# Performance work log

Measured on AMD Instinct MI355X. Metric: run time of the kernel, lower is better.

The kernel has to match this reference:

```python
import jax, jax.numpy as jnp
import numpy as np

N = 40000      # nodes
E = 640000     # edges
F_IN = 128     # feature_dim
HID = 256      # hidden_dim
OUT = 128      # out_dim
B = 64         # num graphs
HEADS = 4
EPS = 1e-5


def setup_inputs() -> dict:
    key = jax.random.key(0)
    ks = jax.random.split(key, 32)
    s = 0.02
    inp = {
        "x_bb_masked": jax.random.normal(ks[0], (N, F_IN), jnp.float32),
        "x_att_masked": jax.random.normal(ks[1], (N, F_IN), jnp.float32),
        # SAGEConv1: in->hid  (lin_l acts on mean-aggregated neighbors, lin_r on root)
        "W1l": jax.random.normal(ks[2], (HID, F_IN), jnp.float32) * s,
        "b1l": jnp.zeros((HID,), jnp.float32),
        "W1r": jax.random.normal(ks[3], (HID, F_IN), jnp.float32) * s,
        # SAGEConv2: hid->hid
        "W2l": jax.random.normal(ks[4], (HID, HID), jnp.float32) * s,
        "b2l": jnp.zeros((HID,), jnp.float32),
        "W2r": jax.random.normal(ks[5], (HID, HID), jnp.float32) * s,
        # SAGEConv3: hid->out
        "W3l": jax.random.normal(ks[6], (OUT, HID), jnp.float32) * s,
        "b3l": jnp.zeros((OUT,), jnp.float32),
        "W3r": jax.random.normal(ks[7], (OUT, HID), jnp.float32) * s,
        # cross-attention projections
        "Wq": jax.random.normal(ks[8], (HID, F_IN), jnp.float32) * s,
        "bq": jnp.zeros((HID,), jnp.float32),
        "Wk": jax.random.normal(ks[9], (HID, OUT), jnp.float32) * s,
        "bk": jnp.zeros((HID,), jnp.float32),
        "Wv": jax.random.normal(ks[10], (HID, OUT), jnp.float32) * s,
        "bv": jnp.zeros((HID,), jnp.float32),
        # nn.MultiheadAttention packed in-proj and out-proj
        "in_proj_w": jax.random.normal(ks[11], (3 * HID, HID), jnp.float32) * s,
        "in_proj_b": jnp.zeros((3 * HID,), jnp.float32),
        "out_w": jax.random.normal(ks[12], (HID, HID), jnp.float32) * s,
        "out_b": jnp.zeros((HID,), jnp.float32),
        "ln_g": jnp.ones((HID,), jnp.float32),
        "ln_b": jnp.zeros((HID,), jnp.float32),
        "edge_index": jax.random.randint(ks[13], (2, E), 0, N, jnp.int64),
        "batch": jnp.sort(jax.random.randint(ks[14], (N,), 0, B, jnp.int64)),
    }
    return inp


def _sage(x, src, dst, Wl, bl, Wr):
    # mean aggregation of source features at target nodes, then lin_l(agg)+lin_r(x)
    agg = jax.ops.segment_sum(x[src], dst, num_segments=N)          # [N, d]
    cnt = jax.ops.segment_sum(jnp.ones((src.shape[0],), x.dtype), dst, num_segments=N)
    mean = agg / jnp.maximum(cnt, 1.0)[:, None]
    return mean @ Wl.T + bl + x @ Wr.T


def _forward(x_bb_masked, x_att_masked,
             W1l, b1l, W1r, W2l, b2l, W2r, W3l, b3l, W3r,
             Wq, bq, Wk, bk, Wv, bv, in_proj_w, in_proj_b, out_w, out_b,
             ln_g, ln_b, edge_index, batch):
    src, dst = edge_index[0], edge_index[1]
    h = jax.nn.relu(_sage(x_bb_masked, src, dst, W1l, b1l, W1r))
    h = jax.nn.relu(_sage(h, src, dst, W2l, b2l, W2r))
    h = _sage(h, src, dst, W3l, b3l, W3r)                           # [N, OUT]
    # global mean pool per graph
    gsum = jax.ops.segment_sum(h, batch, num_segments=B)            # [B, OUT]
    gcnt = jax.ops.segment_sum(jnp.ones((N,), h.dtype), batch, num_segments=B)
    graph_vec = gsum / jnp.maximum(gcnt, 1.0)[:, None]

    # cross attention: query per node, key/value from its graph vector (seq_len = 1)
    query = x_att_masked @ Wq.T + bq                                # [N, HID]
    gv = graph_vec[batch]                                           # [N, OUT]
    keyt = gv @ Wk.T + bk
    val = gv @ Wv.T + bv
    q = query @ in_proj_w[:HID].T + in_proj_b[:HID]
    k = keyt @ in_proj_w[HID:2 * HID].T + in_proj_b[HID:2 * HID]
    v = val @ in_proj_w[2 * HID:].T + in_proj_b[2 * HID:]
    dh = HID // HEADS
    qh = q.reshape(N, HEADS, dh)
    kh = k.reshape(N, HEADS, dh)
    vh = v.reshape(N, HEADS, dh)
    scores = jnp.sum(qh * kh, axis=-1, keepdims=True) / jnp.sqrt(jnp.asarray(dh, q.dtype))
    w = jax.nn.softmax(scores, axis=-1)                             # length-1 kv -> ones
    attn = (w * vh).reshape(N, HID)
    attn = attn @ out_w.T + out_b
    # LayerNorm
    mu = jnp.mean(attn, axis=-1, keepdims=True)
    var = jnp.mean((attn - mu) ** 2, axis=-1, keepdims=True)
    node_embeddings = (attn - mu) / jnp.sqrt(var + EPS) * ln_g + ln_b
    return graph_vec, node_embeddings


def reference(x_bb_masked, x_att_masked,
              W1l, b1l, W1r, W2l, b2l, W2r, W3l, b3l, W3r,
              Wq, bq, Wk, bk, Wv, bv, in_proj_w, in_proj_b, out_w, out_b,
              ln_g, ln_b, edge_index, batch):
    return _forward(x_bb_masked, x_att_masked,
                    W1l, b1l, W1r, W2l, b2l, W2r, W3l, b3l, W3r,
                    Wq, bq, Wk, bk, Wv, bv, in_proj_w, in_proj_b, out_w, out_b,
                    ln_g, ln_b, edge_index, batch)
```

## Files before the change

### kernel.cpp

```cpp
#include <hip/hip_runtime.h>

#define N_NODES 40000
#define N_EDGES 640000
#define NGRAPH 64

typedef unsigned short u16;
typedef unsigned int u32;
typedef __attribute__((ext_vector_type(4))) float floatx4;
typedef __attribute__((ext_vector_type(8))) short short8;
typedef __attribute__((ext_vector_type(8))) __bf16 bf16x8;

__device__ __forceinline__ float bf2f(u16 u) {
  u32 x = ((u32)u) << 16;
  return __builtin_bit_cast(float, x);
}
__device__ __forceinline__ u16 f2bf(float f) {
  u32 u = __builtin_bit_cast(u32, f);
  u += 0x7fffu + ((u >> 16) & 1u);
  return (u16)(u >> 16);
}
__device__ __forceinline__ void gld16(const void* g, void* l) {
  __builtin_amdgcn_global_load_lds(
      (const __attribute__((address_space(1))) u32*)g,
      (__attribute__((address_space(3))) u32*)l, 16, 0, 0);
}

__global__ void k_zero(int* p, int n) {
  int i = blockIdx.x * 256 + threadIdx.x;
  if (i < n) p[i] = 0;
}
__global__ void k_hist(const int* __restrict__ ei, int* __restrict__ cnt) {
  int e = blockIdx.x * 256 + threadIdx.x;
  int d = ei[N_EDGES + e];
  atomicAdd(&cnt[d], 1);
}
__global__ void k_blocksum(const int* __restrict__ cnt, int* __restrict__ bsum, int n) {
  __shared__ int s[256];
  int t = threadIdx.x, i = blockIdx.x * 256 + t;
  s[t] = (i < n) ? cnt[i] : 0;
  __syncthreads();
  for (int off = 128; off > 0; off >>= 1) {
    if (t < off) s[t] += s[t + off];
    __syncthreads();
  }
  if (t == 0) bsum[blockIdx.x] = s[0];
}
__global__ void k_scan_small(int* bsum, int n) {
  __shared__ int s[256];
  int t = threadIdx.x;
  int orig = (t < n) ? bsum[t] : 0;
  s[t] = orig;
  __syncthreads();
  for (int off = 1; off < 256; off <<= 1) {
    int v = (t >= off) ? s[t - off] : 0;
    __syncthreads();
    s[t] += v;
    __syncthreads();
  }
  if (t < n) bsum[t] = s[t] - orig;
}
__global__ void k_rowptr(const int* __restrict__ cnt, const int* __restrict__ bsum,
                         int* __restrict__ rowptr, float* __restrict__ invc, int n, int total) {
  __shared__ int s[256];
  int t = threadIdx.x, i = blockIdx.x * 256 + t;
  int c = (i < n) ? cnt[i] : 0;
  s[t] = c;
  __syncthreads();
  for (int off = 1; off < 256; off <<= 1) {
    int v = (t >= off) ? s[t - off] : 0;
    __syncthreads();
    s[t] += v;
    __syncthreads();
  }
  if (i < n) {
    rowptr[i] = bsum[blockIdx.x] + s[t] - c;
    invc[i] = 1.0f / (float)(c > 1 ? c : 1);
  }
  if (i == 0) rowptr[n] = total;
}
__global__ void k_scatter(const int* __restrict__ ei, const int* __restrict__ rowptr,
                          int* __restrict__ cursor, int* __restrict__ perm) {
  int e = blockIdx.x * 256 + threadIdx.x;
  int d = ei[N_EDGES + e];
  int srcn = ei[e];
  int pos = rowptr[d] + atomicAdd(&cursor[d], 1);
  perm[pos] = srcn;
}
__global__ void k_gstart(const int* __restrict__ batch, int* __restrict__ gstart) {
  int t = threadIdx.x;
  if (t <= NGRAPH) {
    int lo = 0, hi = N_NODES;
    while (lo < hi) { int mid = (lo + hi) >> 1; if (batch[mid] < t) lo = mid + 1; else hi = mid; }
    gstart[t] = lo;
  }
}

__global__ void k_f2b(const float* __restrict__ in, u16* __restrict__ out, int n4) {
  int i = blockIdx.x * 256 + threadIdx.x;
  if (i < n4) {
    float4 v = ((const float4*)in)[i];
    u32 lo = (u32)f2bf(v.x) | ((u32)f2bf(v.y) << 16);
    u32 hi = (u32)f2bf(v.z) | ((u32)f2bf(v.w) << 16);
    ((uint2*)out)[i] = make_uint2(lo, hi);
  }
}
__global__ void k_f2b6(const float* __restrict__ s0, u16* __restrict__ d0,
                       const float* __restrict__ s1, u16* __restrict__ d1,
                       const float* __restrict__ s2, u16* __restrict__ d2,
                       const float* __restrict__ s3, u16* __restrict__ d3,
                       const float* __restrict__ s4, u16* __restrict__ d4,
                       const float* __restrict__ s5, u16* __restrict__ d5) {
  int i = blockIdx.x * 256 + threadIdx.x;
  const float* s; u16* d; int off;
  if (i < 8192)       { s = s0; d = d0; off = i; }
  else if (i < 16384) { s = s1; d = d1; off = i - 8192; }
  else if (i < 32768) { s = s2; d = d2; off = i - 16384; }
  else if (i < 49152) { s = s3; d = d3; off = i - 32768; }
  else if (i < 57344) { s = s4; d = d4; off = i - 49152; }
  else                { s = s5; d = d5; off = i - 57344; }
  float4 v = ((const float4*)s)[off];
  u32 lo = (u32)f2bf(v.x) | ((u32)f2bf(v.y) << 16);
  u32 hi = (u32)f2bf(v.z) | ((u32)f2bf(v.w) << 16);
  ((uint2*)(d))[off] = make_uint2(lo, hi);
}

template <int D, int MODE>
__global__ __launch_bounds__(256) void k_agg(const u16* __restrict__ x, u16* __restrict__ outp,
                                             const int* __restrict__ rowptr,
                                             const int* __restrict__ perm,
                                             const float* __restrict__ invc,
                                             const u16* __restrict__ Radd, int nn) {
  constexpr int CW = D / 2;
  constexpr int LPR = CW / 8;
  constexpr int SLOTS = 64 / LPR;
  int wv = threadIdx.x >> 6, lane = threadIdx.x & 63;
  int node = blockIdx.x * 4 + wv;
  if (node >= nn) return;
  int s = rowptr[node], e = rowptr[node + 1];
  int slot = lane / LPR, lsub = lane % LPR;
  float acc[8];
#pragma unroll
  for (int i = 0; i < 8; ++i) acc[i] = 0.f;
  const u16* xl = x + blockIdx.y * CW + lsub * 8;

  int p = s + slot;
  for (; p + SLOTS < e; p += 2 * SLOTS) {
    int s0 = perm[p], s1 = perm[p + SLOTS];
    uint4 a = *(const uint4*)(xl + (size_t)s0 * D);
    uint4 b = *(const uint4*)(xl + (size_t)s1 * D);
    u32 wa[4] = {a.x, a.y, a.z, a.w}, wb[4] = {b.x, b.y, b.z, b.w};
#pragma unroll
    for (int j = 0; j < 4; ++j) {
      acc[2 * j] += __builtin_bit_cast(float, wa[j] << 16) + __builtin_bit_cast(float, wb[j] << 16);
      acc[2 * j + 1] += __builtin_bit_cast(float, wa[j] & 0xffff0000u) + __builtin_bit_cast(float, wb[j] & 0xffff0000u);
    }
  }
  for (; p < e; p += SLOTS) {
    int src = perm[p];
    uint4 a = *(const uint4*)(xl + (size_t)src * D);
    u32 wa[4] = {a.x, a.y, a.z, a.w};
#pragma unroll
    for (int j = 0; j < 4; ++j) {
      acc[2 * j] += __builtin_bit_cast(float, wa[j] << 16);
      acc[2 * j + 1] += __builtin_bit_cast(float, wa[j] & 0xffff0000u);
    }
  }

#pragma unroll
  for (int i = 0; i < 8; ++i) {
    if (SLOTS == 8) acc[i] += __shfl_xor(acc[i], 8, 64);
    acc[i] += __shfl_xor(acc[i], 16, 64);
    acc[i] += __shfl_xor(acc[i], 32, 64);
  }

  if (slot == 0) {
    float iv = invc[node];
    float v[8];
#pragma unroll
    for (int i = 0; i < 8; ++i) v[i] = acc[i] * iv;
    if (MODE == 1) {
      uint4 a = *(const uint4*)(Radd + (size_t)node * D + blockIdx.y * CW + lsub * 8);
      u32 wa[4] = {a.x, a.y, a.z, a.w};
#pragma unroll
      for (int j = 0; j < 4; ++j) {
        v[2 * j] += __builtin_bit_cast(float, wa[j] << 16);
        v[2 * j + 1] += __builtin_bit_cast(float, wa[j] & 0xffff0000u);
      }
    }
    u32 wpk[4];
#pragma unroll
    for (int i = 0; i < 4; ++i)
      wpk[i] = (u32)f2bf(v[2 * i]) | ((u32)f2bf(v[2 * i + 1]) << 16);
    *(uint4*)(outp + (size_t)node * D + blockIdx.y * CW + lsub * 8) =
        make_uint4(wpk[0], wpk[1], wpk[2], wpk[3]);
  }
}

template <int OUTW, int EPI>
__global__ __launch_bounds__(256) void k_gemm(const u16* __restrict__ A1, const u16* __restrict__ W1, int K1,
                                              const u16* __restrict__ A2, const u16* __restrict__ W2, int K2,
                                              const float* __restrict__ bias,
                                              u16* __restrict__ out1, u16* __restrict__ out2, int M) {
  __shared__ u16 lsA[128 * 64];
  __shared__ u16 lsB[128 * 64];
  const int tid = threadIdx.x, lane = tid & 63, wv = tid >> 6;
  const int wm = wv >> 1, wn = wv & 1;
  const int row0 = blockIdx.x * 128, col0 = blockIdx.y * 128;

  floatx4 acc[4][4];
#pragma unroll
  for (int r = 0; r < 4; ++r)
#pragma unroll
    for (int c = 0; c < 4; ++c) acc[r][c] = 0.f;

  for (int seg = 0; seg < 2; ++seg) {
    const u16* A = seg ? A2 : A1;
    const u16* Wm = seg ? W2 : W1;
    const int K = seg ? K2 : K1;
    if (K == 0) continue;
    for (int k0 = 0; k0 < K; k0 += 64) {
      __syncthreads();
#pragma unroll
      for (int i = 0; i < 4; ++i) {
        int chunk = i * 256 + tid;
        int r = chunk >> 3;
        int kc = chunk & 7;
        int kcs = kc ^ (r & 7);
        int grow = row0 + r;
        grow = grow < M ? grow : M - 1;
        gld16(A + (size_t)grow * K + (k0 + kcs * 8), lsA + (size_t)(i * 256 + wv * 64) * 8);
        int wr = col0 + r;
        gld16(Wm + (size_t)wr * K + (k0 + kcs * 8), lsB + (size_t)(i * 256 + wv * 64) * 8);
      }
      __syncthreads();
#pragma unroll
      for (int kk = 0; kk < 2; ++kk) {
        bf16x8 af[4], bb[4];
        int kc = kk * 4 + (lane >> 4);
#pragma unroll
        for (int r = 0; r < 4; ++r) {
          int row = wm * 64 + r * 16 + (lane & 15);
          af[r] = __builtin_bit_cast(bf16x8, *(const short8*)(lsA + row * 64 + ((kc ^ (row & 7)) << 3)));
        }
#pragma unroll
        for (int c = 0; c < 4; ++c) {
          int row = wn * 64 + c * 16 + (lane & 15);
          bb[c] = __builtin_bit_cast(bf16x8, *(const short8*)(lsB + row * 64 + ((kc ^ (row & 7)) << 3)));
        }
#pragma unroll
        for (int r = 0; r < 4; ++r)
#pragma unroll
          for (int c = 0; c < 4; ++c)
            acc[r][c] = __builtin_amdgcn_mfma_f32_16x16x32_bf16(af[r], bb[c], acc[r][c], 0, 0, 0);
      }
    }
  }

#pragma unroll
  for (int r = 0; r < 4; ++r) {
    int rowb = row0 + wm * 64 + r * 16 + ((lane >> 4) << 2);
#pragma unroll
    for (int c = 0; c < 4; ++c) {
      int col = col0 + wn * 64 + c * 16 + (lane & 15);
#pragma unroll
      for (int j = 0; j < 4; ++j) {
        int gr = rowb + j;
        if (gr < M) {
          float v = acc[r][c][j];
          if (EPI == 0) {
            v += bias[col];
            v = v > 0.f ? v : 0.f;
            out1[(size_t)gr * OUTW + col] = f2bf(v);
          } else {
            if (col < 128) {
              out1[(size_t)gr * 128 + col] = f2bf(v);
            } else {
              v += bias[col - 128];
              out2[(size_t)gr * 128 + (col - 128)] = f2bf(v);
            }
          }
        }
      }
    }
  }
}

__global__ __launch_bounds__(256) void k_pool_part(const u16* __restrict__ h3,
                                                   const int* __restrict__ batch,
                                                   float* __restrict__ gsum) {
  __shared__ int sb[64];
  int t = threadIdx.x;
  int n0 = blockIdx.x * 64;
  if (t < 64) sb[t] = batch[n0 + t];
  __syncthreads();
  int col = t & 127, sub = t >> 7;
  float acc = 0.f;
  int curg = -1;
  for (int i = sub; i < 64; i += 2) {
    int g = sb[i];
    if (g != curg) {
      if (curg >= 0) atomicAdd(&gsum[curg * 128 + col], acc);
      curg = g;
      acc = 0.f;
    }
    acc += bf2f(h3[(size_t)(n0 + i) * 128 + col]);
  }
  if (curg >= 0) atomicAdd(&gsum[curg * 128 + col], acc);
}

__global__ __launch_bounds__(256) void k_tail(const float* __restrict__ gsum, const int* __restrict__ gstart,
                                              const float* __restrict__ Wv,
                                              const float* __restrict__ bv, const float* __restrict__ ipw,
                                              const float* __restrict__ ipb, const float* __restrict__ outw,
                                              const float* __restrict__ outb, const float* __restrict__ lng,
                                              const float* __restrict__ lnb, float* __restrict__ dout,
                                              float* __restrict__ eout) {
  __shared__ float sa[256], sb[256];
  __shared__ float s_mu, s_var;
  int b = blockIdx.x, t = threadIdx.x;
  if (t < 128) {
    int cg = gstart[b + 1] - gstart[b];
    float mean = gsum[b * 128 + t] / (float)(cg > 1 ? cg : 1);
    sa[t] = mean;
    dout[b * 128 + t] = mean;
  }
  __syncthreads();
  float val = bv[t];
  for (int k = 0; k < 128; ++k) val += sa[k] * Wv[t * 128 + k];
  sb[t] = val;
  __syncthreads();
  float vv = ipb[512 + t];
  for (int k = 0; k < 256; ++k) vv += sb[k] * ipw[(size_t)(512 + t) * 256 + k];
  sa[t] = vv;
  __syncthreads();
  float at = outb[t];
  for (int k = 0; k < 256; ++k) at += sa[k] * outw[t * 256 + k];
  sb[t] = at;
  __syncthreads();
  for (int off = 128; off > 0; off >>= 1) {
    if (t < off) sb[t] += sb[t + off];
    __syncthreads();
  }
  if (t == 0) s_mu = sb[0] * (1.0f / 256.0f);
  __syncthreads();
  float d = at - s_mu;
  sb[t] = d * d;
  __syncthreads();
  for (int off = 128; off > 0; off >>= 1) {
    if (t < off) sb[t] += sb[t + off];
    __syncthreads();
  }
  if (t == 0) s_var = sb[0] * (1.0f / 256.0f);
  __syncthreads();
  float r = 1.0f / sqrtf(s_var + 1e-5f);
  eout[(size_t)b * 256 + t] = d * r * lng[t] + lnb[t];
}

__global__ void k_scat_out(const float* __restrict__ eb, const int* __restrict__ batch,
                           float* __restrict__ dout) {
  int i = blockIdx.x * 256 + threadIdx.x;
  int n = i >> 6, q = i & 63;
  float4 v = ((const float4*)eb)[(size_t)batch[n] * 64 + q];
  ((float4*)(dout + NGRAPH * 128))[i] = v;
}

extern "C" void kernel_launch(void* const* d_in, const int* in_sizes, int n_in,
                              void* d_out, int out_size, void* d_ws, size_t ws_size,
                              hipStream_t stream) {
  (void)in_sizes; (void)n_in; (void)out_size; (void)ws_size;
  const float* x_bb = (const float*)d_in[0];
  const float* W1l = (const float*)d_in[2];
  const float* b1l = (const float*)d_in[3];
  const float* W1r = (const float*)d_in[4];
  const float* W2l = (const float*)d_in[5];
  const float* b2l = (const float*)d_in[6];
  const float* W2r = (const float*)d_in[7];
  const float* W3l = (const float*)d_in[8];
  const float* b3l = (const float*)d_in[9];
  const float* W3r = (const float*)d_in[10];
  const float* Wv = (const float*)d_in[15];
  const float* bv = (const float*)d_in[16];
  const float* ipw = (const float*)d_in[17];
  const float* ipb = (const float*)d_in[18];
  const float* outw = (const float*)d_in[19];
  const float* outb = (const float*)d_in[20];
  const float* lng = (const float*)d_in[21];
  const float* lnb = (const float*)d_in[22];
  const int* ei = (const int*)d_in[23];
  const int* batch = (const int*)d_in[24];
  float* dout = (float*)d_out;
  char* ws = (char*)d_ws;

  constexpr size_t O_W1L = 0;
  constexpr size_t O_W1R = O_W1L + 256 * 128 * 2;
  constexpr size_t O_W2L = O_W1R + 256 * 128 * 2;
  constexpr size_t O_W2R = O_W2L + 256 * 256 * 2;
  constexpr size_t O_W3L = O_W2R + 256 * 256 * 2;
  constexpr size_t O_W3R = O_W3L + 128 * 256 * 2;
  constexpr size_t O_XB = O_W3R + 128 * 256 * 2;
  constexpr size_t O_MEAN1 = O_XB + (size_t)N_NODES * 128 * 2;
  constexpr size_t O_H1 = O_MEAN1 + (size_t)N_NODES * 128 * 2;
  constexpr size_t O_MEAN2 = O_H1 + (size_t)N_NODES * 256 * 2;
  constexpr size_t O_H2 = O_MEAN2 + (size_t)N_NODES * 256 * 2;
  constexpr size_t O_E = O_H2 + (size_t)N_NODES * 256 * 2;
  constexpr size_t O_CNT = O_E + 64 * 256 * 4;
  constexpr size_t O_CUR = O_CNT + (size_t)N_NODES * 4;
  constexpr size_t O_GSUM = O_CUR + (size_t)N_NODES * 4;
  constexpr size_t O_RP = O_GSUM + 64 * 128 * 4;
  constexpr size_t O_INVC = O_RP + (size_t)(N_NODES + 64) * 4;
  constexpr size_t O_BSUM = O_INVC + (size_t)N_NODES * 4;
  constexpr size_t O_GST = O_BSUM + 1024;
  constexpr size_t O_PERM = O_GST + 512;

  u16* w1l = (u16*)(ws + O_W1L);  u16* w1r = (u16*)(ws + O_W1R);
  u16* w2l = (u16*)(ws + O_W2L);  u16* w2r = (u16*)(ws + O_W2R);
  u16* w3s = (u16*)(ws + O_W3L);  u16* w3r = (u16*)(ws + O_W3R);
  u16* xb = (u16*)(ws + O_XB);
  u16* mean1 = (u16*)(ws + O_MEAN1);
  u16* h1 = (u16*)(ws + O_H1);
  u16* mean2 = (u16*)(ws + O_MEAN2);
  u16* h2 = (u16*)(ws + O_H2);
  u16* Pb = (u16*)(ws + O_XB);
  u16* Rb = (u16*)(ws + O_MEAN1);
  u16* h3b = (u16*)(ws + O_MEAN2);
  float* eb = (float*)(ws + O_E);
  int* cnt = (int*)(ws + O_CNT);
  int* cursor = (int*)(ws + O_CUR);
  float* gsum = (float*)(ws + O_GSUM);
  int* rowptr = (int*)(ws + O_RP);
  float* invc = (float*)(ws + O_INVC);
  int* bsum = (int*)(ws + O_BSUM);
  int* gstart = (int*)(ws + O_GST);
  int* perm = (int*)(ws + O_PERM);

  const int NB = (N_NODES + 255) / 256;

  k_zero<<<(2 * N_NODES + 8192 + 255) / 256, 256, 0, stream>>>(cnt, 2 * N_NODES + 8192);
  k_hist<<<N_EDGES / 256, 256, 0, stream>>>(ei, cnt);
  k_blocksum<<<NB, 256, 0, stream>>>(cnt, bsum, N_NODES);
  k_scan_small<<<1, 256, 0, stream>>>(bsum, NB);
  k_rowptr<<<NB, 256, 0, stream>>>(cnt, bsum, rowptr, invc, N_NODES, N_EDGES);
  k_scatter<<<N_EDGES / 256, 256, 0, stream>>>(ei, rowptr, cursor, perm);
  k_gstart<<<1, 128, 0, stream>>>(batch, gstart);

  k_f2b<<<(N_NODES * 128 / 4 + 255) / 256, 256, 0, stream>>>(x_bb, xb, N_NODES * 128 / 4);
  k_f2b6<<<256, 256, 0, stream>>>(W1l, w1l, W1r, w1r, W2l, w2l, W2r, w2r, W3l, w3s, W3r, w3r);

  dim3 blk(256);
  dim3 gagg(N_NODES / 4, 2);
  k_agg<128, 0><<<gagg, blk, 0, stream>>>(xb, mean1, rowptr, perm, invc, nullptr, N_NODES);
  k_gemm<256, 0><<<dim3(313, 2), blk, 0, stream>>>(mean1, w1l, 128, xb, w1r, 128, b1l, h1, nullptr, N_NODES);
  k_agg<256, 0><<<gagg, blk, 0, stream>>>(h1, mean2, rowptr, perm, invc, nullptr, N_NODES);
  k_gemm<256, 0><<<dim3(313, 2), blk, 0, stream>>>(mean2, w2l, 256, h1, w2r, 256, b2l, h2, nullptr, N_NODES);
  k_gemm<128, 3><<<dim3(313, 2), blk, 0, stream>>>(h2, w3s, 256, nullptr, nullptr, 0, b3l, Pb, Rb, N_NODES);
  k_agg<128, 1><<<gagg, blk, 0, stream>>>(Pb, h3b, rowptr, perm, invc, Rb, N_NODES);
  k_pool_part<<<N_NODES / 64, blk, 0, stream>>>(h3b, batch, gsum);
  k_tail<<<NGRAPH, blk, 0, stream>>>(gsum, gstart, Wv, bv, ipw, ipb, outw, outb, lng, lnb, dout, eb);
  k_scat_out<<<N_NODES * 64 / 256, blk, 0, stream>>>(eb, batch, dout);
}
```

Before: 317.0 us.

## Fuse preprocessing and tail stages into cooperative grid-synced kernels; widen agg rows

Replaces the chain of small CSR-build and conversion kernels with one cooperative kernel that uses grid-wide syncs between phases. Pool, tail MLP/LayerNorm and output scatter are likewise merged into a single cooperative kernel. The aggregation kernel now has one wave cover the full feature row (16 lanes per row, 4 edge slots) instead of splitting columns across a second grid dimension, which halves the number of index loads per row. The aim is to cut launch overhead and redundant perm reads, at the cost of grid.sync overhead and a fixed 512-block grid.

```diff
diff --git a/kernel.cpp b/kernel.cpp
--- a/kernel.cpp
+++ b/kernel.cpp
@@ -1,8 +1,12 @@
 #include <hip/hip_runtime.h>
+#include <hip/hip_cooperative_groups.h>
+
+namespace cg = cooperative_groups;
 
 #define N_NODES 40000
 #define N_EDGES 640000
 #define NGRAPH 64
+#define NBCH 157
 
 typedef unsigned short u16;
 typedef unsigned int u32;
@@ -19,109 +23,102 @@
   u += 0x7fffu + ((u >> 16) & 1u);
   return (u16)(u >> 16);
 }
+__device__ __forceinline__ uint2 f4tob(float4 v) {
+  u32 lo = (u32)f2bf(v.x) | ((u32)f2bf(v.y) << 16);
+  u32 hi = (u32)f2bf(v.z) | ((u32)f2bf(v.w) << 16);
+  return make_uint2(lo, hi);
+}
 __device__ __forceinline__ void gld16(const void* g, void* l) {
   __builtin_amdgcn_global_load_lds(
       (const __attribute__((address_space(1))) u32*)g,
       (__attribute__((address_space(3))) u32*)l, 16, 0, 0);
 }
 
-__global__ void k_zero(int* p, int n) {
-  int i = blockIdx.x * 256 + threadIdx.x;
-  if (i < n) p[i] = 0;
-}
-__global__ void k_hist(const int* __restrict__ ei, int* __restrict__ cnt) {
-  int e = blockIdx.x * 256 + threadIdx.x;
-  int d = ei[N_EDGES + e];
-  atomicAdd(&cnt[d], 1);
-}
-__global__ void k_blocksum(const int* __restrict__ cnt, int* __restrict__ bsum, int n) {
-  __shared__ int s[256];
-  int t = threadIdx.x, i = blockIdx.x * 256 + t;
-  s[t] = (i < n) ? cnt[i] : 0;
-  __syncthreads();
-  for (int off = 128; off > 0; off >>= 1) {
-    if (t < off) s[t] += s[t + off];
-    __syncthreads();
-  }
-  if (t == 0) bsum[blockIdx.x] = s[0];
-}
-__global__ void k_scan_small(int* bsum, int n) {
-  __shared__ int s[256];
-  int t = threadIdx.x;
-  int orig = (t < n) ? bsum[t] : 0;
-  s[t] = orig;
-  __syncthreads();
-  for (int off = 1; off < 256; off <<= 1) {
-    int v = (t >= off) ? s[t - off] : 0;
-    __syncthreads();
-    s[t] += v;
-    __syncthreads();
-  }
-  if (t < n) bsum[t] = s[t] - orig;
-}
-__global__ void k_rowptr(const int* __restrict__ cnt, const int* __restrict__ bsum,
-                         int* __restrict__ rowptr, float* __restrict__ invc, int n, int total) {
-  __shared__ int s[256];
-  int t = threadIdx.x, i = blockIdx.x * 256 + t;
-  int c = (i < n) ? cnt[i] : 0;
-  s[t] = c;
-  __syncthreads();
-  for (int off = 1; off < 256; off <<= 1) {
-    int v = (t >= off) ? s[t - off] : 0;
-    __syncthreads();
-    s[t] += v;
-    __syncthreads();
-  }
-  if (i < n) {
-    rowptr[i] = bsum[blockIdx.x] + s[t] - c;
-    invc[i] = 1.0f / (float)(c > 1 ? c : 1);
-  }
-  if (i == 0) rowptr[n] = total;
-}
-__global__ void k_scatter(const int* __restrict__ ei, const int* __restrict__ rowptr,
-                          int* __restrict__ cursor, int* __restrict__ perm) {
-  int e = blockIdx.x * 256 + threadIdx.x;
-  int d = ei[N_EDGES + e];
-  int srcn = ei[e];
-  int pos = rowptr[d] + atomicAdd(&cursor[d], 1);
-  perm[pos] = srcn;
-}
-__global__ void k_gstart(const int* __restrict__ batch, int* __restrict__ gstart) {
-  int t = threadIdx.x;
-  if (t <= NGRAPH) {
+struct PreArgs {
+  const float* x_bb;
+  const float *W1l, *W1r, *W2l, *W2r, *W3l, *W3r;
+  const int* ei;
+  const int* batch;
+  u16 *xb, *w1l, *w1r, *w2l, *w2r, *w3s, *w3r;
+  int* cnt;
+  int* cursor;
+  int* rowptr;
+  float* invc;
+  int* bsum;
+  int* gstart;
+  int* perm;
+};
+
+__global__ __launch_bounds__(256, 4) void k_pre(PreArgs a) {
+  cg::grid_group grid = cg::this_grid();
+  __shared__ int ssc[256];
+  const int t = threadIdx.x;
+  const int tid = blockIdx.x * 256 + t;
+  const int nth = gridDim.x * 256;
+
+  for (int i = tid; i < 2 * N_NODES + 8192; i += nth) a.cnt[i] = 0;
+  for (int i = tid; i < N_NODES * 32; i += nth)
+    ((uint2*)a.xb)[i] = f4tob(((const float4*)a.x_bb)[i]);
+  for (int i = tid; i < 65536; i += nth) {
+    const float* s; u16* d; int off;
+    if (i < 8192)       { s = a.W1l; d = a.w1l; off = i; }
+    else if (i < 16384) { s = a.W1r; d = a.w1r; off = i - 8192; }
+    else if (i < 32768) { s = a.W2l; d = a.w2l; off = i - 16384; }
+    else if (i < 49152) { s = a.W2r; d = a.w2r; off = i - 32768; }
+    else if (i < 57344) { s = a.W3l; d = a.w3s; off = i - 49152; }
+    else                { s = a.W3r; d = a.w3r; off = i - 57344; }
+    ((uint2*)d)[off] = f4tob(((const float4*)s)[off]);
+  }
+  grid.sync();
+  for (int e2 = tid; e2 < N_EDGES; e2 += nth)
+    atomicAdd(&a.cnt[a.ei[N_EDGES + e2]], 1);
+  grid.sync();
+  for (int c = blockIdx.x; c < NBCH; c += gridDim.x) {
+    int i = c * 256 + t;
+    int cv = (i < N_NODES) ? a.cnt[i] : 0;
+    ssc[t] = cv;
+    __syncthreads();
+    for (int off = 1; off < 256; off <<= 1) {
+      int v = (t >= off) ? ssc[t - off] : 0;
+      __syncthreads();
+      ssc[t] += v;
+      __syncthreads();
+    }
+    if (i < N_NODES) a.rowptr[i] = ssc[t] - cv;
+    if (t == 255) a.bsum[c] = ssc[255];
+    __syncthreads();
+  }
+  grid.sync();
+  if (blockIdx.x == 0) {
+    int orig = (t < NBCH) ? a.bsum[t] : 0;
+    ssc[t] = orig;
+    __syncthreads();
+    for (int off = 1; off < 256; off <<= 1) {
+      int v = (t >= off) ? ssc[t - off] : 0;
+      __syncthreads();
+      ssc[t] += v;
+      __syncthreads();
+    }
+    if (t < NBCH) a.bsum[t] = ssc[t] - orig;
+  }
+  grid.sync();
+  for (int i = tid; i < N_NODES; i += nth) {
+    int cv = a.cnt[i];
+    a.rowptr[i] += a.bsum[i >> 8];
+    a.invc[i] = 1.0f / (float)(cv > 1 ? cv : 1);
+  }
+  if (tid == 0) a.rowptr[N_NODES] = N_EDGES;
+  grid.sync();
+  for (int e2 = tid; e2 < N_EDGES; e2 += nth) {
+    int d = a.ei[N_EDGES + e2];
+    int pos = a.rowptr[d] + atomicAdd(&a.cursor[d], 1);
+    a.perm[pos] = a.ei[e2];
+  }
+  if (tid <= NGRAPH) {
     int lo = 0, hi = N_NODES;
-    while (lo < hi) { int mid = (lo + hi) >> 1; if (batch[mid] < t) lo = mid + 1; else hi = mid; }
-    gstart[t] = lo;
-  }
-}
-
-__global__ void k_f2b(const float* __restrict__ in, u16* __restrict__ out, int n4) {
-  int i = blockIdx.x * 256 + threadIdx.x;
-  if (i < n4) {
-    float4 v = ((const float4*)in)[i];
-    u32 lo = (u32)f2bf(v.x) | ((u32)f2bf(v.y) << 16);
-    u32 hi = (u32)f2bf(v.z) | ((u32)f2bf(v.w) << 16);
-    ((uint2*)out)[i] = make_uint2(lo, hi);
-  }
-}
-__global__ void k_f2b6(const float* __restrict__ s0, u16* __restrict__ d0,
-                       const float* __restrict__ s1, u16* __restrict__ d1,
-                       const float* __restrict__ s2, u16* __restrict__ d2,
-                       const float* __restrict__ s3, u16* __restrict__ d3,
-                       const float* __restrict__ s4, u16* __restrict__ d4,
-                       const float* __restrict__ s5, u16* __restrict__ d5) {
-  int i = blockIdx.x * 256 + threadIdx.x;
-  const float* s; u16* d; int off;
-  if (i < 8192)       { s = s0; d = d0; off = i; }
-  else if (i < 16384) { s = s1; d = d1; off = i - 8192; }
-  else if (i < 32768) { s = s2; d = d2; off = i - 16384; }
-  else if (i < 49152) { s = s3; d = d3; off = i - 32768; }
-  else if (i < 57344) { s = s4; d = d4; off = i - 49152; }
-  else                { s = s5; d = d5; off = i - 57344; }
-  float4 v = ((const float4*)s)[off];
-  u32 lo = (u32)f2bf(v.x) | ((u32)f2bf(v.y) << 16);
-  u32 hi = (u32)f2bf(v.z) | ((u32)f2bf(v.w) << 16);
-  ((uint2*)(d))[off] = make_uint2(lo, hi);
+    while (lo < hi) { int mid = (lo + hi) >> 1; if (a.batch[mid] < tid) lo = mid + 1; else hi = mid; }
+    a.gstart[tid] = lo;
+  }
 }
 
 template <int D, int MODE>
@@ -130,69 +127,97 @@
                                              const int* __restrict__ perm,
                                              const float* __restrict__ invc,
                                              const u16* __restrict__ Radd, int nn) {
-  constexpr int CW = D / 2;
-  constexpr int LPR = CW / 8;
-  constexpr int SLOTS = 64 / LPR;
   int wv = threadIdx.x >> 6, lane = threadIdx.x & 63;
   int node = blockIdx.x * 4 + wv;
   if (node >= nn) return;
   int s = rowptr[node], e = rowptr[node + 1];
-  int slot = lane / LPR, lsub = lane % LPR;
-  float acc[8];
-#pragma unroll
-  for (int i = 0; i < 8; ++i) acc[i] = 0.f;
-  const u16* xl = x + blockIdx.y * CW + lsub * 8;
+  int slot = lane >> 4, lsub = lane & 15;
+  constexpr int FR = D / 16;
+  float acc[FR];
+#pragma unroll
+  for (int i = 0; i < FR; ++i) acc[i] = 0.f;
+  const u16* xl = x + lsub * FR;
 
   int p = s + slot;
-  for (; p + SLOTS < e; p += 2 * SLOTS) {
-    int s0 = perm[p], s1 = perm[p + SLOTS];
-    uint4 a = *(const uint4*)(xl + (size_t)s0 * D);
-    uint4 b = *(const uint4*)(xl + (size_t)s1 * D);
-    u32 wa[4] = {a.x, a.y, a.z, a.w}, wb[4] = {b.x, b.y, b.z, b.w};
-#pragma unroll
-    for (int j = 0; j < 4; ++j) {
-      acc[2 * j] += __builtin_bit_cast(float, wa[j] << 16) + __builtin_bit_cast(float, wb[j] << 16);
-      acc[2 * j + 1] += __builtin_bit_cast(float, wa[j] & 0xffff0000u) + __builtin_bit_cast(float, wb[j] & 0xffff0000u);
-    }
-  }
-  for (; p < e; p += SLOTS) {
+  for (; p + 4 < e; p += 8) {
+    int src0 = perm[p];
+    int src1 = perm[p + 4];
+    const u16* rp0 = xl + (size_t)src0 * D;
+    const u16* rp1 = xl + (size_t)src1 * D;
+    if (D == 128) {
+      uint4 va = *(const uint4*)rp0;
+      uint4 vb = *(const uint4*)rp1;
+      u32 wa[4] = {va.x, va.y, va.z, va.w}, wb[4] = {vb.x, vb.y, vb.z, vb.w};
+#pragma unroll
+      for (int j = 0; j < 4; ++j) {
+        acc[2 * j] += __builtin_bit_cast(float, wa[j] << 16) + __builtin_bit_cast(float, wb[j] << 16);
+        acc[2 * j + 1] += __builtin_bit_cast(float, wa[j] & 0xffff0000u) + __builtin_bit_cast(float, wb[j] & 0xffff0000u);
+      }
+    } else {
+      uint4 a0 = *(const uint4*)rp0;
+      uint4 a1 = *(const uint4*)(rp0 + 8);
+      uint4 b0 = *(const uint4*)rp1;
+      uint4 b1 = *(const uint4*)(rp1 + 8);
+      u32 wa[8] = {a0.x, a0.y, a0.z, a0.w, a1.x, a1.y, a1.z, a1.w};
+      u32 wb[8] = {b0.x, b0.y, b0.z, b0.w, b1.x, b1.y, b1.z, b1.w};
+#pragma unroll
+      for (int j = 0; j < 8; ++j) {
+        acc[2 * j] += __builtin_bit_cast(float, wa[j] << 16) + __builtin_bit_cast(float, wb[j] << 16);
+        acc[2 * j + 1] += __builtin_bit_cast(float, wa[j] & 0xffff0000u) + __builtin_bit_cast(float, wb[j] & 0xffff0000u);
+      }
+    }
+  }
+  if (p < e) {
     int src = perm[p];
-    uint4 a = *(const uint4*)(xl + (size_t)src * D);
-    u32 wa[4] = {a.x, a.y, a.z, a.w};
-#pragma unroll
-    for (int j = 0; j < 4; ++j) {
-      acc[2 * j] += __builtin_bit_cast(float, wa[j] << 16);
-      acc[2 * j + 1] += __builtin_bit_cast(float, wa[j] & 0xffff0000u);
-    }
-  }
-
-#pragma unroll
-  for (int i = 0; i < 8; ++i) {
-    if (SLOTS == 8) acc[i] += __shfl_xor(acc[i], 8, 64);
+    const u16* rp = xl + (size_t)src * D;
+    if (D == 128) {
+      uint4 va = *(const uint4*)rp;
+      u32 wa[4] = {va.x, va.y, va.z, va.w};
+#pragma unroll
+      for (int j = 0; j < 4; ++j) {
+        acc[2 * j] += __builtin_bit_cast(float, wa[j] << 16);
+        acc[2 * j + 1] += __builtin_bit_cast(float, wa[j] & 0xffff0000u);
+      }
+    } else {
+      uint4 a0 = *(const uint4*)rp;
+      uint4 a1 = *(const uint4*)(rp + 8);
+      u32 wa[8] = {a0.x, a0.y, a0.z, a0.w, a1.x, a1.y, a1.z, a1.w};
+#pragma unroll
+      for (int j = 0; j < 8; ++j) {
+        acc[2 * j] += __builtin_bit_cast(float, wa[j] << 16);
+        acc[2 * j + 1] += __builtin_bit_cast(float, wa[j] & 0xffff0000u);
+      }
+    }
+  }
+
+#pragma unroll
+  for (int i = 0; i < FR; ++i) {
     acc[i] += __shfl_xor(acc[i], 16, 64);
     acc[i] += __shfl_xor(acc[i], 32, 64);
   }
 
   if (slot == 0) {
     float iv = invc[node];
-    float v[8];
-#pragma unroll
-    for (int i = 0; i < 8; ++i) v[i] = acc[i] * iv;
+    float v[FR];
+#pragma unroll
+    for (int i = 0; i < FR; ++i) v[i] = acc[i] * iv;
     if (MODE == 1) {
-      uint4 a = *(const uint4*)(Radd + (size_t)node * D + blockIdx.y * CW + lsub * 8);
-      u32 wa[4] = {a.x, a.y, a.z, a.w};
+      const uint4* rr = (const uint4*)(Radd + (size_t)node * D + lsub * FR);
+      uint4 va = rr[0];
+      u32 wa[4] = {va.x, va.y, va.z, va.w};
 #pragma unroll
       for (int j = 0; j < 4; ++j) {
         v[2 * j] += __builtin_bit_cast(float, wa[j] << 16);
         v[2 * j + 1] += __builtin_bit_cast(float, wa[j] & 0xffff0000u);
       }
     }
-    u32 wpk[4];
-#pragma unroll
-    for (int i = 0; i < 4; ++i)
+    u32 wpk[FR / 2];
+#pragma unroll
+    for (int i = 0; i < FR / 2; ++i)
       wpk[i] = (u32)f2bf(v[2 * i]) | ((u32)f2bf(v[2 * i + 1]) << 16);
-    *(uint4*)(outp + (size_t)node * D + blockIdx.y * CW + lsub * 8) =
-        make_uint4(wpk[0], wpk[1], wpk[2], wpk[3]);
+    uint4* o = (uint4*)(outp + (size_t)node * D + lsub * FR);
+    o[0] = make_uint4(wpk[0], wpk[1], wpk[2], wpk[3]);
+    if (FR == 16) o[1] = make_uint4(wpk[4], wpk[5], wpk[6], wpk[7]);
   }
 }
 
@@ -285,83 +310,89 @@
   }
 }
 
-__global__ __launch_bounds__(256) void k_pool_part(const u16* __restrict__ h3,
-                                                   const int* __restrict__ batch,
-                                                   float* __restrict__ gsum) {
-  __shared__ int sb[64];
-  int t = threadIdx.x;
-  int n0 = blockIdx.x * 64;
-  if (t < 64) sb[t] = batch[n0 + t];
-  __syncthreads();
-  int col = t & 127, sub = t >> 7;
-  float acc = 0.f;
-  int curg = -1;
-  for (int i = sub; i < 64; i += 2) {
-    int g = sb[i];
-    if (g != curg) {
-      if (curg >= 0) atomicAdd(&gsum[curg * 128 + col], acc);
-      curg = g;
-      acc = 0.f;
-    }
-    acc += bf2f(h3[(size_t)(n0 + i) * 128 + col]);
-  }
-  if (curg >= 0) atomicAdd(&gsum[curg * 128 + col], acc);
-}
-
-__global__ __launch_bounds__(256) void k_tail(const float* __restrict__ gsum, const int* __restrict__ gstart,
-                                              const float* __restrict__ Wv,
-                                              const float* __restrict__ bv, const float* __restrict__ ipw,
-                                              const float* __restrict__ ipb, const float* __restrict__ outw,
-                                              const float* __restrict__ outb, const float* __restrict__ lng,
-                                              const float* __restrict__ lnb, float* __restrict__ dout,
-                                              float* __restrict__ eout) {
+struct PostArgs {
+  const u16* h3;
+  const int* batch;
+  float* gsum;
+  const int* gstart;
+  const float *Wv, *bv, *ipw, *ipb, *outw, *outb, *lng, *lnb;
+  float* dout;
+  float* eout;
+};
+
+__global__ __launch_bounds__(256, 4) void k_post(PostArgs a) {
+  cg::grid_group grid = cg::this_grid();
   __shared__ float sa[256], sb[256];
+  __shared__ int sbi[64];
   __shared__ float s_mu, s_var;
-  int b = blockIdx.x, t = threadIdx.x;
-  if (t < 128) {
-    int cg = gstart[b + 1] - gstart[b];
-    float mean = gsum[b * 128 + t] / (float)(cg > 1 ? cg : 1);
-    sa[t] = mean;
-    dout[b * 128 + t] = mean;
-  }
-  __syncthreads();
-  float val = bv[t];
-  for (int k = 0; k < 128; ++k) val += sa[k] * Wv[t * 128 + k];
-  sb[t] = val;
-  __syncthreads();
-  float vv = ipb[512 + t];
-  for (int k = 0; k < 256; ++k) vv += sb[k] * ipw[(size_t)(512 + t) * 256 + k];
-  sa[t] = vv;
-  __syncthreads();
-  float at = outb[t];
-  for (int k = 0; k < 256; ++k) at += sa[k] * outw[t * 256 + k];
-  sb[t] = at;
-  __syncthreads();
-  for (int off = 128; off > 0; off >>= 1) {
-    if (t < off) sb[t] += sb[t + off];
-    __syncthreads();
-  }
-  if (t == 0) s_mu = sb[0] * (1.0f / 256.0f);
-  __syncthreads();
-  float d = at - s_mu;
-  sb[t] = d * d;
-  __syncthreads();
-  for (int off = 128; off > 0; off >>= 1) {
-    if (t < off) sb[t] += sb[t + off];
-    __syncthreads();
-  }
-  if (t == 0) s_var = sb[0] * (1.0f / 256.0f);
-  __syncthreads();
-  float r = 1.0f / sqrtf(s_var + 1e-5f);
-  eout[(size_t)b * 256 + t] = d * r * lng[t] + lnb[t];
-}
-
-__global__ void k_scat_out(const float* __restrict__ eb, const int* __restrict__ batch,
-                           float* __restrict__ dout) {
-  int i = blockIdx.x * 256 + threadIdx.x;
-  int n = i >> 6, q = i & 63;
-  float4 v = ((const float4*)eb)[(size_t)batch[n] * 64 + q];
-  ((float4*)(dout + NGRAPH * 128))[i] = v;
+  const int t = threadIdx.x;
+
+  for (int c = blockIdx.x; c < N_NODES / 64; c += gridDim.x) {
+    int n0 = c * 64;
+    if (t < 64) sbi[t] = a.batch[n0 + t];
+    __syncthreads();
+    int col = t & 127, sub = t >> 7;
+    float acc = 0.f;
+    int curg = -1;
+    for (int i = sub; i < 64; i += 2) {
+      int g = sbi[i];
+      if (g != curg) {
+        if (curg >= 0) atomicAdd(&a.gsum[curg * 128 + col], acc);
+        curg = g;
+        acc = 0.f;
+      }
+      acc += bf2f(a.h3[(size_t)(n0 + i) * 128 + col]);
+    }
+    if (curg >= 0) atomicAdd(&a.gsum[curg * 128 + col], acc);
+    __syncthreads();
+  }
+  grid.sync();
+  if (blockIdx.x < NGRAPH) {
+    int b = blockIdx.x;
+    if (t < 128) {
+      int cg2 = a.gstart[b + 1] - a.gstart[b];
+      float mean = a.gsum[b * 128 + t] / (float)(cg2 > 1 ? cg2 : 1);
+      sa[t] = mean;
+      a.dout[b * 128 + t] = mean;
+    }
+    __syncthreads();
+    float val = a.bv[t];
+    for (int k = 0; k < 128; ++k) val += sa[k] * a.Wv[t * 128 + k];
+    sb[t] = val;
+    __syncthreads();
+    float vv = a.ipb[512 + t];
+    for (int k = 0; k < 256; ++k) vv += sb[k] * a.ipw[(size_t)(512 + t) * 256 + k];
+    sa[t] = vv;
+    __syncthreads();
+    float at = a.outb[t];
+    for (int k = 0; k < 256; ++k) at += sa[k] * a.outw[t * 256 + k];
+    sb[t] = at;
+    __syncthreads();
+    for (int off = 128; off > 0; off >>= 1) {
+      if (t < off) sb[t] += sb[t + off];
+      __syncthreads();
+    }
+    if (t == 0) s_mu = sb[0] * (1.0f / 256.0f);
+    __syncthreads();
+    float d = at - s_mu;
+    sb[t] = d * d;
+    __syncthreads();
+    for (int off = 128; off > 0; off >>= 1) {
+      if (t < off) sb[t] += sb[t + off];
+      __syncthreads();
+    }
+    if (t == 0) s_var = sb[0] * (1.0f / 256.0f);
+    __syncthreads();
+    float r = 1.0f / sqrtf(s_var + 1e-5f);
+    a.eout[(size_t)b * 256 + t] = d * r * a.lng[t] + a.lnb[t];
+  }
+  grid.sync();
+  const int nth = gridDim.x * 256;
+  float4* od = (float4*)(a.dout + NGRAPH * 128);
+  for (int i = blockIdx.x * 256 + t; i < N_NODES * 64; i += nth) {
+    int n = i >> 6, q = i & 63;
+    od[i] = ((const float4*)a.eout)[(size_t)a.batch[n] * 64 + q];
+  }
 }
 
 extern "C" void kernel_launch(void* const* d_in, const int* in_sizes, int n_in,
@@ -433,28 +464,29 @@
   int* gstart = (int*)(ws + O_GST);
   int* perm = (int*)(ws + O_PERM);
 
-  const int NB = (N_NODES + 255) / 256;
-
-  k_zero<<<(2 * N_NODES + 8192 + 255) / 256, 256, 0, stream>>>(cnt, 2 * N_NODES + 8192);
-  k_hist<<<N_EDGES / 256, 256, 0, stream>>>(ei, cnt);
-  k_blocksum<<<NB, 256, 0, stream>>>(cnt, bsum, N_NODES);
-  k_scan_small<<<1, 256, 0, stream>>>(bsum, NB);
-  k_rowptr<<<NB, 256, 0, stream>>>(cnt, bsum, rowptr, invc, N_NODES, N_EDGES);
-  k_scatter<<<N_EDGES / 256, 256, 0, stream>>>(ei, rowptr, cursor, perm);
-  k_gstart<<<1, 128, 0, stream>>>(batch, gstart);
-
-  k_f2b<<<(N_NODES * 128 / 4 + 255) / 256, 256, 0, stream>>>(x_bb, xb, N_NODES * 128 / 4);
-  k_f2b6<<<256, 256, 0, stream>>>(W1l, w1l, W1r, w1r, W2l, w2l, W2r, w2r, W3l, w3s, W3r, w3r);
+  PreArgs pa;
+  pa.x_bb = x_bb; pa.W1l = W1l; pa.W1r = W1r; pa.W2l = W2l; pa.W2r = W2r;
+  pa.W3l = W3l; pa.W3r = W3r; pa.ei = ei; pa.batch = batch;
+  pa.xb = xb; pa.w1l = w1l; pa.w1r = w1r; pa.w2l = w2l; pa.w2r = w2r;
+  pa.w3s = w3s; pa.w3r = w3r;
+  pa.cnt = cnt; pa.cursor = cursor; pa.rowptr = rowptr; pa.invc = invc;
+  pa.bsum = bsum; pa.gstart = gstart; pa.perm = perm;
+  void* pargs[] = { &pa };
+  hipLaunchCooperativeKernel((void*)k_pre, dim3(512), dim3(256), pargs, 0, stream);
 
   dim3 blk(256);
-  dim3 gagg(N_NODES / 4, 2);
-  k_agg<128, 0><<<gagg, blk, 0, stream>>>(xb, mean1, rowptr, perm, invc, nullptr, N_NODES);
+  k_agg<128, 0><<<N_NODES / 4, blk, 0, stream>>>(xb, mean1, rowptr, perm, invc, nullptr, N_NODES);
   k_gemm<256, 0><<<dim3(313, 2), blk, 0, stream>>>(mean1, w1l, 128, xb, w1r, 128, b1l, h1, nullptr, N_NODES);
-  k_agg<256, 0><<<gagg, blk, 0, stream>>>(h1, mean2, rowptr, perm, invc, nullptr, N_NODES);
+  k_agg<256, 0><<<N_NODES / 4, blk, 0, stream>>>(h1, mean2, rowptr, perm, invc, nullptr, N_NODES);
   k_gemm<256, 0><<<dim3(313, 2), blk, 0, stream>>>(mean2, w2l, 256, h1, w2r, 256, b2l, h2, nullptr, N_NODES);
   k_gemm<128, 3><<<dim3(313, 2), blk, 0, stream>>>(h2, w3s, 256, nullptr, nullptr, 0, b3l, Pb, Rb, N_NODES);
-  k_agg<128, 1><<<gagg, blk, 0, stream>>>(Pb, h3b, rowptr, perm, invc, Rb, N_NODES);
-  k_pool_part<<<N_NODES / 64, blk, 0, stream>>>(h3b, batch, gsum);
-  k_tail<<<NGRAPH, blk, 0, stream>>>(gsum, gstart, Wv, bv, ipw, ipb, outw, outb, lng, lnb, dout, eb);
-  k_scat_out<<<N_NODES * 64 / 256, blk, 0, stream>>>(eb, batch, dout);
-}
+  k_agg<128, 1><<<N_NODES / 4, blk, 0, stream>>>(Pb, h3b, rowptr, perm, invc, Rb, N_NODES);
+
+  PostArgs qa;
+  qa.h3 = h3b; qa.batch = batch; qa.gsum = gsum; qa.gstart = gstart;
+  qa.Wv = Wv; qa.bv = bv; qa.ipw = ipw; qa.ipb = ipb;
+  qa.outw = outw; qa.outb = outb; qa.lng = lng; qa.lnb = lnb;
+  qa.dout = dout; qa.eout = eb;
+  void* qargs[] = { &qa };
+  hipLaunchCooperativeKernel((void*)k_post, dim3(512), dim3(256), qargs, 0, stream);
+}
```

Result: slower. 697.5 us (+120.1%).

## Merge setup kernels and process full feature rows per wave in aggregation

Applied to the files above, without the earlier changes.

Folds the zeroing, bf16 conversion of x and weights, and graph-start search into a single grid-stride setup kernel, cutting several launches. The aggregation kernel drops the two-way column split in blockIdx.y: each wave now covers the whole feature row with 16 lanes per row and 4 edge slots, loading 16 or 32 bytes per lane. Each edge index is read once instead of twice and the block count halves. The trade-off is fewer waves and more registers for the D=256 case, plus only 4 edges in flight per wave where D=128 previously had 8.

```diff
diff --git a/kernel.cpp b/kernel.cpp
--- a/kernel.cpp
+++ b/kernel.cpp
@@ -19,16 +19,48 @@
   u += 0x7fffu + ((u >> 16) & 1u);
   return (u16)(u >> 16);
 }
+__device__ __forceinline__ uint2 f4tob(float4 v) {
+  u32 lo = (u32)f2bf(v.x) | ((u32)f2bf(v.y) << 16);
+  u32 hi = (u32)f2bf(v.z) | ((u32)f2bf(v.w) << 16);
+  return make_uint2(lo, hi);
+}
 __device__ __forceinline__ void gld16(const void* g, void* l) {
   __builtin_amdgcn_global_load_lds(
       (const __attribute__((address_space(1))) u32*)g,
       (__attribute__((address_space(3))) u32*)l, 16, 0, 0);
 }
 
-__global__ void k_zero(int* p, int n) {
-  int i = blockIdx.x * 256 + threadIdx.x;
-  if (i < n) p[i] = 0;
-}
+__global__ __launch_bounds__(256) void k_setup(const float* __restrict__ x_bb, u16* __restrict__ xb,
+                                               const float* __restrict__ W1l, u16* __restrict__ w1l,
+                                               const float* __restrict__ W1r, u16* __restrict__ w1r,
+                                               const float* __restrict__ W2l, u16* __restrict__ w2l,
+                                               const float* __restrict__ W2r, u16* __restrict__ w2r,
+                                               const float* __restrict__ W3l, u16* __restrict__ w3s,
+                                               const float* __restrict__ W3r, u16* __restrict__ w3r,
+                                               int* __restrict__ zbase,
+                                               const int* __restrict__ batch, int* __restrict__ gstart) {
+  const int tid = blockIdx.x * 256 + threadIdx.x;
+  const int nth = gridDim.x * 256;
+  for (int i = tid; i < 2 * N_NODES + 8192; i += nth) zbase[i] = 0;
+  for (int i = tid; i < N_NODES * 32; i += nth)
+    ((uint2*)xb)[i] = f4tob(((const float4*)x_bb)[i]);
+  for (int i = tid; i < 65536; i += nth) {
+    const float* s; u16* d; int off;
+    if (i < 8192)       { s = W1l; d = w1l; off = i; }
+    else if (i < 16384) { s = W1r; d = w1r; off = i - 8192; }
+    else if (i < 32768) { s = W2l; d = w2l; off = i - 16384; }
+    else if (i < 49152) { s = W2r; d = w2r; off = i - 32768; }
+    else if (i < 57344) { s = W3l; d = w3s; off = i - 49152; }
+    else                { s = W3r; d = w3r; off = i - 57344; }
+    ((uint2*)d)[off] = f4tob(((const float4*)s)[off]);
+  }
+  if (tid <= NGRAPH) {
+    int lo = 0, hi = N_NODES;
+    while (lo < hi) { int mid = (lo + hi) >> 1; if (batch[mid] < tid) lo = mid + 1; else hi = mid; }
+    gstart[tid] = lo;
+  }
+}
+
 __global__ void k_hist(const int* __restrict__ ei, int* __restrict__ cnt) {
   int e = blockIdx.x * 256 + threadIdx.x;
   int d = ei[N_EDGES + e];
@@ -86,43 +118,6 @@
   int pos = rowptr[d] + atomicAdd(&cursor[d], 1);
   perm[pos] = srcn;
 }
-__global__ void k_gstart(const int* __restrict__ batch, int* __restrict__ gstart) {
-  int t = threadIdx.x;
-  if (t <= NGRAPH) {
-    int lo = 0, hi = N_NODES;
-    while (lo < hi) { int mid = (lo + hi) >> 1; if (batch[mid] < t) lo = mid + 1; else hi = mid; }
-    gstart[t] = lo;
-  }
-}
-
-__global__ void k_f2b(const float* __restrict__ in, u16* __restrict__ out, int n4) {
-  int i = blockIdx.x * 256 + threadIdx.x;
-  if (i < n4) {
-    float4 v = ((const float4*)in)[i];
-    u32 lo = (u32)f2bf(v.x) | ((u32)f2bf(v.y) << 16);
-    u32 hi = (u32)f2bf(v.z) | ((u32)f2bf(v.w) << 16);
-    ((uint2*)out)[i] = make_uint2(lo, hi);
-  }
-}
-__global__ void k_f2b6(const float* __restrict__ s0, u16* __restrict__ d0,
-                       const float* __restrict__ s1, u16* __restrict__ d1,
-                       const float* __restrict__ s2, u16* __restrict__ d2,
-                       const float* __restrict__ s3, u16* __restrict__ d3,
-                       const float* __restrict__ s4, u16* __restrict__ d4,
-                       const float* __restrict__ s5, u16* __restrict__ d5) {
-  int i = blockIdx.x * 256 + threadIdx.x;
-  const float* s; u16* d; int off;
-  if (i < 8192)       { s = s0; d = d0; off = i; }
-  else if (i < 16384) { s = s1; d = d1; off = i - 8192; }
-  else if (i < 32768) { s = s2; d = d2; off = i - 16384; }
-  else if (i < 49152) { s = s3; d = d3; off = i - 32768; }
-  else if (i < 57344) { s = s4; d = d4; off = i - 49152; }
-  else                { s = s5; d = d5; off = i - 57344; }
-  float4 v = ((const float4*)s)[off];
-  u32 lo = (u32)f2bf(v.x) | ((u32)f2bf(v.y) << 16);
-  u32 hi = (u32)f2bf(v.z) | ((u32)f2bf(v.w) << 16);
-  ((uint2*)(d))[off] = make_uint2(lo, hi);
-}
 
 template <int D, int MODE>
 __global__ __launch_bounds__(256) void k_agg(const u16* __restrict__ x, u16* __restrict__ outp,
@@ -130,69 +125,97 @@
                                              const int* __restrict__ perm,
                                              const float* __restrict__ invc,
                                              const u16* __restrict__ Radd, int nn) {
-  constexpr int CW = D / 2;
-  constexpr int LPR = CW / 8;
-  constexpr int SLOTS = 64 / LPR;
   int wv = threadIdx.x >> 6, lane = threadIdx.x & 63;
   int node = blockIdx.x * 4 + wv;
   if (node >= nn) return;
   int s = rowptr[node], e = rowptr[node + 1];
-  int slot = lane / LPR, lsub = lane % LPR;
-  float acc[8];
-#pragma unroll
-  for (int i = 0; i < 8; ++i) acc[i] = 0.f;
-  const u16* xl = x + blockIdx.y * CW + lsub * 8;
+  int slot = lane >> 4, lsub = lane & 15;
+  constexpr int FR = D / 16;
+  float acc[FR];
+#pragma unroll
+  for (int i = 0; i < FR; ++i) acc[i] = 0.f;
+  const u16* xl = x + lsub * FR;
 
   int p = s + slot;
-  for (; p + SLOTS < e; p += 2 * SLOTS) {
-    int s0 = perm[p], s1 = perm[p + SLOTS];
-    uint4 a = *(const uint4*)(xl + (size_t)s0 * D);
-    uint4 b = *(const uint4*)(xl + (size_t)s1 * D);
-    u32 wa[4] = {a.x, a.y, a.z, a.w}, wb[4] = {b.x, b.y, b.z, b.w};
-#pragma unroll
-    for (int j = 0; j < 4; ++j) {
-      acc[2 * j] += __builtin_bit_cast(float, wa[j] << 16) + __builtin_bit_cast(float, wb[j] << 16);
-      acc[2 * j + 1] += __builtin_bit_cast(float, wa[j] & 0xffff0000u) + __builtin_bit_cast(float, wb[j] & 0xffff0000u);
-    }
-  }
-  for (; p < e; p += SLOTS) {
+  for (; p + 4 < e; p += 8) {
+    int src0 = perm[p];
+    int src1 = perm[p + 4];
+    const u16* rp0 = xl + (size_t)src0 * D;
+    const u16* rp1 = xl + (size_t)src1 * D;
+    if (D == 128) {
+      uint4 va = *(const uint4*)rp0;
+      uint4 vb = *(const uint4*)rp1;
+      u32 wa[4] = {va.x, va.y, va.z, va.w}, wb[4] = {vb.x, vb.y, vb.z, vb.w};
+#pragma unroll
+      for (int j = 0; j < 4; ++j) {
+        acc[2 * j] += __builtin_bit_cast(float, wa[j] << 16) + __builtin_bit_cast(float, wb[j] << 16);
+        acc[2 * j + 1] += __builtin_bit_cast(float, wa[j] & 0xffff0000u) + __builtin_bit_cast(float, wb[j] & 0xffff0000u);
+      }
+    } else {
+      uint4 a0 = *(const uint4*)rp0;
+      uint4 a1 = *(const uint4*)(rp0 + 8);
+      uint4 b0 = *(const uint4*)rp1;
+      uint4 b1 = *(const uint4*)(rp1 + 8);
+      u32 wa[8] = {a0.x, a0.y, a0.z, a0.w, a1.x, a1.y, a1.z, a1.w};
+      u32 wb[8] = {b0.x, b0.y, b0.z, b0.w, b1.x, b1.y, b1.z, b1.w};
+#pragma unroll
+      for (int j = 0; j < 8; ++j) {
+        acc[2 * j] += __builtin_bit_cast(float, wa[j] << 16) + __builtin_bit_cast(float, wb[j] << 16);
+        acc[2 * j + 1] += __builtin_bit_cast(float, wa[j] & 0xffff0000u) + __builtin_bit_cast(float, wb[j] & 0xffff0000u);
+      }
+    }
+  }
+  if (p < e) {
     int src = perm[p];
-    uint4 a = *(const uint4*)(xl + (size_t)src * D);
-    u32 wa[4] = {a.x, a.y, a.z, a.w};
-#pragma unroll
-    for (int j = 0; j < 4; ++j) {
-      acc[2 * j] += __builtin_bit_cast(float, wa[j] << 16);
-      acc[2 * j + 1] += __builtin_bit_cast(float, wa[j] & 0xffff0000u);
-    }
-  }
-
-#pragma unroll
-  for (int i = 0; i < 8; ++i) {
-    if (SLOTS == 8) acc[i] += __shfl_xor(acc[i], 8, 64);
+    const u16* rp = xl + (size_t)src * D;
+    if (D == 128) {
+      uint4 va = *(const uint4*)rp;
+      u32 wa[4] = {va.x, va.y, va.z, va.w};
+#pragma unroll
+      for (int j = 0; j < 4; ++j) {
+        acc[2 * j] += __builtin_bit_cast(float, wa[j] << 16);
+        acc[2 * j + 1] += __builtin_bit_cast(float, wa[j] & 0xffff0000u);
+      }
+    } else {
+      uint4 a0 = *(const uint4*)rp;
+      uint4 a1 = *(const uint4*)(rp + 8);
+      u32 wa[8] = {a0.x, a0.y, a0.z, a0.w, a1.x, a1.y, a1.z, a1.w};
+#pragma unroll
+      for (int j = 0; j < 8; ++j) {
+        acc[2 * j] += __builtin_bit_cast(float, wa[j] << 16);
+        acc[2 * j + 1] += __builtin_bit_cast(float, wa[j] & 0xffff0000u);
+      }
+    }
+  }
+
+#pragma unroll
+  for (int i = 0; i < FR; ++i) {
     acc[i] += __shfl_xor(acc[i], 16, 64);
     acc[i] += __shfl_xor(acc[i], 32, 64);
   }
 
   if (slot == 0) {
     float iv = invc[node];
-    float v[8];
-#pragma unroll
-    for (int i = 0; i < 8; ++i) v[i] = acc[i] * iv;
+    float v[FR];
+#pragma unroll
+    for (int i = 0; i < FR; ++i) v[i] = acc[i] * iv;
     if (MODE == 1) {
-      uint4 a = *(const uint4*)(Radd + (size_t)node * D + blockIdx.y * CW + lsub * 8);
-      u32 wa[4] = {a.x, a.y, a.z, a.w};
+      const uint4* rr = (const uint4*)(Radd + (size_t)node * D + lsub * FR);
+      uint4 va = rr[0];
+      u32 wa[4] = {va.x, va.y, va.z, va.w};
 #pragma unroll
       for (int j = 0; j < 4; ++j) {
         v[2 * j] += __builtin_bit_cast(float, wa[j] << 16);
         v[2 * j + 1] += __builtin_bit_cast(float, wa[j] & 0xffff0000u);
       }
     }
-    u32 wpk[4];
-#pragma unroll
-    for (int i = 0; i < 4; ++i)
+    u32 wpk[FR / 2];
+#pragma unroll
+    for (int i = 0; i < FR / 2; ++i)
       wpk[i] = (u32)f2bf(v[2 * i]) | ((u32)f2bf(v[2 * i + 1]) << 16);
-    *(uint4*)(outp + (size_t)node * D + blockIdx.y * CW + lsub * 8) =
-        make_uint4(wpk[0], wpk[1], wpk[2], wpk[3]);
+    uint4* o = (uint4*)(outp + (size_t)node * D + lsub * FR);
+    o[0] = make_uint4(wpk[0], wpk[1], wpk[2], wpk[3]);
+    if (FR == 16) o[1] = make_uint4(wpk[4], wpk[5], wpk[6], wpk[7]);
   }
 }
 
@@ -434,26 +457,23 @@
   int* perm = (int*)(ws + O_PERM);
 
   const int NB = (N_NODES + 255) / 256;
-
-  k_zero<<<(2 * N_NODES + 8192 + 255) / 256, 256, 0, stream>>>(cnt, 2 * N_NODES + 8192);
-  k_hist<<<N_EDGES / 256, 256, 0, stream>>>(ei, cnt);
-  k_blocksum<<<NB, 256, 0, stream>>>(cnt, bsum, N_NODES);
-  k_scan_small<<<1, 256, 0, stream>>>(bsum, NB);
-  k_rowptr<<<NB, 256, 0, stream>>>(cnt, bsum, rowptr, invc, N_NODES, N_EDGES);
-  k_scatter<<<N_EDGES / 256, 256, 0, stream>>>(ei, rowptr, cursor, perm);
-  k_gstart<<<1, 128, 0, stream>>>(batch, gstart);
-
-  k_f2b<<<(N_NODES * 128 / 4 + 255) / 256, 256, 0, stream>>>(x_bb, xb, N_NODES * 128 / 4);
-  k_f2b6<<<256, 256, 0, stream>>>(W1l, w1l, W1r, w1r, W2l, w2l, W2r, w2r, W3l, w3s, W3r, w3r);
-
   dim3 blk(256);
-  dim3 gagg(N_NODES / 4, 2);
-  k_agg<128, 0><<<gagg, blk, 0, stream>>>(xb, mean1, rowptr, perm, invc, nullptr, N_NODES);
+
+  k_setup<<<512, blk, 0, stream>>>(x_bb, xb, W1l, w1l, W1r, w1r, W2l, w2l, W2r, w2r,
+                                   W3l, w3s, W3r, w3r, cnt, batch, gstart);
+  k_hist<<<N_EDGES / 256, blk, 0, stream>>>(ei, cnt);
+  k_blocksum<<<NB, blk, 0, stream>>>(cnt, bsum, N_NODES);
+  k_scan_small<<<1, blk, 0, stream>>>(bsum, NB);
+  k_rowptr<<<NB, blk, 0, stream>>>(cnt, bsum, rowptr, invc, N_NODES, N_EDGES);
+  k_scatter<<<N_EDGES / 256, blk, 0, stream>>>(ei, rowptr, cursor, perm);
+
+  k_agg<128, 0><<<N_NODES / 4, blk, 0, stream>>>(xb, mean1, rowptr, perm, invc, nullptr, N_NODES);
   k_gemm<256, 0><<<dim3(313, 2), blk, 0, stream>>>(mean1, w1l, 128, xb, w1r, 128, b1l, h1, nullptr, N_NODES);
-  k_agg<256, 0><<<gagg, blk, 0, stream>>>(h1, mean2, rowptr, perm, invc, nullptr, N_NODES);
+  k_agg<256, 0><<<N_NODES / 4, blk, 0, stream>>>(h1, mean2, rowptr, perm, invc, nullptr, N_NODES);
   k_gemm<256, 0><<<dim3(313, 2), blk, 0, stream>>>(mean2, w2l, 256, h1, w2r, 256, b2l, h2, nullptr, N_NODES);
   k_gemm<128, 3><<<dim3(313, 2), blk, 0, stream>>>(h2, w3s, 256, nullptr, nullptr, 0, b3l, Pb, Rb, N_NODES);
-  k_agg<128, 1><<<gagg, blk, 0, stream>>>(Pb, h3b, rowptr, perm, invc, Rb, N_NODES);
+  k_agg<128, 1><<<N_NODES / 4, blk, 0, stream>>>(Pb, h3b, rowptr, perm, invc, Rb, N_NODES);
+
   k_pool_part<<<N_NODES / 64, blk, 0, stream>>>(h3b, batch, gsum);
   k_tail<<<NGRAPH, blk, 0, stream>>>(gsum, gstart, Wv, bv, ipw, ipb, outw, outb, lng, lnb, dout, eb);
   k_scat_out<<<N_NODES * 64 / 256, blk, 0, stream>>>(eb, batch, dout);
```

After: 284.7 us. 1.11x faster.
